# Performance work log

Measured on AMD Instinct MI355X. Metric: run time of the kernel, lower is better.

Reference implementation:

```python
import jax, jax.numpy as jnp
import numpy as np

B, S, H = 4, 2048, 1024
NH, HD = 16, 64  # num heads, head dim

def setup_inputs() -> dict:
    key = jax.random.key(0)
    ks = jax.random.split(key, 4)
    scale = 1.0 / np.sqrt(H)
    return {
        "hidden_states": jax.random.normal(ks[0], (B, S, H), dtype=jnp.float32),
        "attention_mask": jnp.zeros((B, 1, 1, S), dtype=jnp.float32),
        "wq": jax.random.normal(ks[1], (H, H), dtype=jnp.float32) * scale,
        "bq": jnp.zeros((H,), dtype=jnp.float32),
        "wk": jax.random.normal(ks[2], (H, H), dtype=jnp.float32) * scale,
        "bk": jnp.zeros((H,), dtype=jnp.float32),
        "wv": jax.random.normal(ks[3], (H, H), dtype=jnp.float32) * scale,
        "bv": jnp.zeros((H,), dtype=jnp.float32),
    }

def _split_heads(x):
    # [B,S,H] -> [B,NH,S,HD]
    return x.reshape(B, S, NH, HD).transpose(0, 2, 1, 3)

def reference(hidden_states, attention_mask, wq, bq, wk, bk, wv, bv):
    # torch F.linear: x @ W^T + b
    q = _split_heads(hidden_states @ wq.T + bq)
    k = _split_heads(hidden_states @ wk.T + bk)
    v = _split_heads(hidden_states @ wv.T + bv)
    scores = jnp.einsum("bhqd,bhkd->bhqk", q, k) / np.sqrt(HD)
    scores = scores + attention_mask  # additive mask, broadcast [B,1,1,S]
    probs = jax.nn.softmax(scores, axis=-1)  # dropout p=0.0 (eval)
    ctx = jnp.einsum("bhqk,bhkd->bhqd", probs, v)
    # [B,NH,S,HD] -> [B,S,H]
    return ctx.transpose(0, 2, 1, 3).reshape(B, S, H)
```

## Files before the change

kernel.cpp:

```cpp
#include <hip/hip_runtime.h>

typedef unsigned short u16;
typedef unsigned int u32;
typedef __bf16 bf16;
typedef bf16 bf16x8 __attribute__((ext_vector_type(8)));
typedef float f32x4 __attribute__((ext_vector_type(4)));
typedef float f32x16 __attribute__((ext_vector_type(16)));
typedef u16 u16x8 __attribute__((ext_vector_type(8)));
typedef u16 u16x4 __attribute__((ext_vector_type(4)));
typedef u32 u32x4 __attribute__((ext_vector_type(4)));

#define B_ 4
#define S_ 2048
#define H_ 1024
#define NH_ 16
#define HD_ 64
#define M_TOT (B_ * S_)
#define N_TOT (3 * H_)

#if __has_builtin(__builtin_amdgcn_exp2f)
#define EXP2(x) __builtin_amdgcn_exp2f(x)
#else
#define EXP2(x) exp2f(x)
#endif

__device__ __forceinline__ u16 f2bf(float f) {
    union { float f; unsigned u; } v; v.f = f;
    unsigned r = v.u + 0x7FFFu + ((v.u >> 16) & 1u);
    return (u16)(r >> 16);
}

__device__ __forceinline__ u32 cvt_pk_bf16(float a, float b) {
    u32 r;
    asm("v_cvt_pk_bf16_f32 %0, %1, %2" : "=v"(r) : "v"(a), "v"(b));
    return r;
}
__device__ __forceinline__ void perm32swap(u32& a, u32& b) {
    asm volatile("v_permlane32_swap_b32 %0, %1" : "+v"(a), "+v"(b));
}

__global__ __launch_bounds__(256) void cvt_bf16(const float* __restrict__ src,
                                                u16* __restrict__ dst, int n4) {
    int i = blockIdx.x * blockDim.x + threadIdx.x;
    int stride = gridDim.x * blockDim.x;
    for (; i < n4; i += stride) {
        float4 v = ((const float4*)src)[i];
        u16 o0 = f2bf(v.x), o1 = f2bf(v.y), o2 = f2bf(v.z), o3 = f2bf(v.w);
        u16* p = dst + i * 4;
        p[0] = o0; p[1] = o1; p[2] = o2; p[3] = o3;
    }
}

__global__ __launch_bounds__(256) void qkv_gemm(
    const u16* __restrict__ X, const u16* __restrict__ W,
    const float* __restrict__ bq, const float* __restrict__ bk, const float* __restrict__ bv,
    u16* __restrict__ Q, u16* __restrict__ Ko, u16* __restrict__ Vt) {
    __shared__ __align__(16) u16 As[128 * 32];
    __shared__ __align__(16) u16 Bs[128 * 32];

    const int tid = threadIdx.x;
    const int lane = tid & 63;
    const int wave = tid >> 6;
    const int m0 = blockIdx.y * 128;
    const int n0 = blockIdx.x * 128;
    const int wr = (wave >> 1) * 64;
    const int wc = (wave & 1) * 64;

    f32x4 acc[4][4];
#pragma unroll
    for (int m = 0; m < 4; m++)
#pragma unroll
        for (int n = 0; n < 4; n++) acc[m][n] = (f32x4){0.f, 0.f, 0.f, 0.f};

    const int ci = wave * 64 + lane;
    const int ra = ci >> 2, ca = (ci & 3) * 8;
    const u16* gA0 = &X[(size_t)(m0 + ra) * H_ + ca];
    const u16* gA1 = &X[(size_t)(m0 + ra + 64) * H_ + ca];
    const u16* gB0 = &W[(size_t)(n0 + ra) * H_ + ca];
    const u16* gB1 = &W[(size_t)(n0 + ra + 64) * H_ + ca];
    char* lA0 = (char*)As + wave * 1024;
    char* lA1 = (char*)As + 4096 + wave * 1024;
    char* lB0 = (char*)Bs + wave * 1024;
    char* lB1 = (char*)Bs + 4096 + wave * 1024;

    const int row_a = lane & 15;
    const int ko = (lane >> 4) * 8;

    for (int k0 = 0; k0 < H_; k0 += 32) {
        __syncthreads();
        __builtin_amdgcn_global_load_lds((const __attribute__((address_space(1))) void*)(gA0 + k0),
                                         (__attribute__((address_space(3))) void*)lA0, 16, 0, 0);
        __builtin_amdgcn_global_load_lds((const __attribute__((address_space(1))) void*)(gA1 + k0),
                                         (__attribute__((address_space(3))) void*)lA1, 16, 0, 0);
        __builtin_amdgcn_global_load_lds((const __attribute__((address_space(1))) void*)(gB0 + k0),
                                         (__attribute__((address_space(3))) void*)lB0, 16, 0, 0);
        __builtin_amdgcn_global_load_lds((const __attribute__((address_space(1))) void*)(gB1 + k0),
                                         (__attribute__((address_space(3))) void*)lB1, 16, 0, 0);
        __syncthreads();

        bf16x8 a[4], bfr[4];
#pragma unroll
        for (int m = 0; m < 4; m++)
            a[m] = *(const bf16x8*)&As[(wr + m * 16 + row_a) * 32 + ko];
#pragma unroll
        for (int n = 0; n < 4; n++)
            bfr[n] = *(const bf16x8*)&Bs[(wc + n * 16 + row_a) * 32 + ko];
#pragma unroll
        for (int m = 0; m < 4; m++)
#pragma unroll
            for (int n = 0; n < 4; n++)
                acc[m][n] = __builtin_amdgcn_mfma_f32_16x16x32_bf16(a[m], bfr[n], acc[m][n], 0, 0, 0);
    }

    const float QS = 0.125f * 1.44269504f;
#pragma unroll
    for (int n = 0; n < 4; n++) {
        int ng = n0 + wc + n * 16 + (lane & 15);
        int which = ng >> 10;
        int nn = ng & 1023;
        const float* bp = (which == 0) ? bq : (which == 1) ? bk : bv;
        float bias = bp[nn];
        float scale = (which == 0) ? QS : 1.0f;
        int h = nn >> 6, d = nn & 63;
#pragma unroll
        for (int m = 0; m < 4; m++) {
            int mg0 = m0 + wr + m * 16 + (lane >> 4) * 4;
            if (which == 2) {
                u16x4 pack;
#pragma unroll
                for (int j = 0; j < 4; j++) pack[j] = f2bf(acc[m][n][j] + bias);
                int bb = mg0 >> 11, s = mg0 & 2047;
                *(u16x4*)&Vt[((((size_t)bb * NH_ + h) * HD_) + d) * S_ + s] = pack;
            } else {
                u16* dst = (which == 0) ? Q : Ko;
#pragma unroll
                for (int j = 0; j < 4; j++) {
                    int mg = mg0 + j;
                    int bb = mg >> 11, s = mg & 2047;
                    float v = (acc[m][n][j] + bias) * scale;
                    dst[((((size_t)bb * NH_ + h) * S_) + s) * HD_ + d] = f2bf(v);
                }
            }
        }
    }
}

#define KVB 64

__global__ __launch_bounds__(256, 4) void attn(
    const u16* __restrict__ Q, const u16* __restrict__ K, const u16* __restrict__ Vt,
    const float* __restrict__ mask, float* __restrict__ out) {
    const int head = blockIdx.y;
    const int b = head >> 4, h = head & 15;
    const int q0 = blockIdx.x * 128;
    const int tid = threadIdx.x;
    const int lane = tid & 63;
    const int wave = tid >> 6;
    const int l31 = lane & 31;
    const int hi = lane >> 5;

    const u16* Qh = Q + (size_t)head * S_ * HD_;
    const u16* Kh = K + (size_t)head * S_ * HD_;
    const u16* Vh = Vt + (size_t)head * HD_ * S_;

    __shared__ __align__(16) u16 Kl[KVB * HD_];
    __shared__ __align__(16) u16 Vl[HD_ * KVB];
    __shared__ __align__(16) float ml[S_];
    __shared__ int snz;

    if (tid == 0) snz = 0;
    __syncthreads();
    {
        int nz = 0;
        const float4* m4 = (const float4*)(mask + (size_t)b * S_);
        for (int i = tid; i < S_ / 4; i += 256) {
            float4 v = m4[i];
            nz |= (v.x != 0.f) | (v.y != 0.f) | (v.z != 0.f) | (v.w != 0.f);
            f32x4 sv = { v.x * 1.44269504f, v.y * 1.44269504f,
                         v.z * 1.44269504f, v.w * 1.44269504f };
            *(f32x4*)&ml[i * 4] = sv;
        }
        if (__any(nz) && lane == 0) atomicOr(&snz, 1);
    }
    __syncthreads();
    const bool mz = (snz == 0);

    bf16x8 qf[4];
    {
        const u16* qp = &Qh[(size_t)(q0 + wave * 32 + l31) * HD_ + hi * 8];
        qf[0] = *(const bf16x8*)(qp);
        qf[1] = *(const bf16x8*)(qp + 16);
        qf[2] = *(const bf16x8*)(qp + 32);
        qf[3] = *(const bf16x8*)(qp + 48);
    }

    f32x16 oacc[2];
#pragma unroll
    for (int dh = 0; dh < 2; dh++)
#pragma unroll
        for (int i = 0; i < 16; i++) oacc[dh][i] = 0.f;
    float m = -1e30f, l = 0.f;

    const int sr = tid >> 2;
    const u32 sdB = (u32)((tid & 3) * 32);
    const u32 swzS = (u32)((sr & 7) << 4);
    const u32 off0 = ((u32)(sr * 128) + sdB) ^ swzS;
    const u32 off1 = off0 ^ 16u;
    const u16* kSrc = &Kh[(size_t)sr * HD_ + (tid & 3) * 16];
    const u16* vSrc = &Vh[(size_t)sr * S_ + (tid & 3) * 16];
    const u32 swzR = (u32)((l31 & 7) << 4);
    const u32 rowB = (u32)(l31 * 128);

    for (int kv0 = 0; kv0 < S_; kv0 += KVB) {
        __syncthreads();
        {
            const u16* ks = kSrc + (size_t)kv0 * HD_;
            const u16* vs = vSrc + kv0;
            u16x8 a0 = *(const u16x8*)ks;
            u16x8 a1 = *(const u16x8*)(ks + 8);
            u16x8 b0 = *(const u16x8*)vs;
            u16x8 b1 = *(const u16x8*)(vs + 8);
            *(u16x8*)((char*)Kl + off0) = a0;
            *(u16x8*)((char*)Kl + off1) = a1;
            *(u16x8*)((char*)Vl + off0) = b0;
            *(u16x8*)((char*)Vl + off1) = b1;
        }
        __syncthreads();

        f32x16 sc[2];
#pragma unroll
        for (int g = 0; g < 2; g++) {
            f32x16 c;
#pragma unroll
            for (int i = 0; i < 16; i++) c[i] = 0.f;
#pragma unroll
            for (int dk = 0; dk < 4; dk++) {
                bf16x8 kf = *(const bf16x8*)((const char*)Kl + g * 4096 + rowB +
                                             (((u32)(dk * 32 + hi * 16)) ^ swzR));
                c = __builtin_amdgcn_mfma_f32_32x32x16_bf16(kf, qf[dk], c, 0, 0, 0);
            }
            sc[g] = c;
        }

        if (!mz) {
#pragma unroll
            for (int g = 0; g < 2; g++)
#pragma unroll
                for (int c4 = 0; c4 < 4; c4++) {
                    f32x4 mk = *(const f32x4*)&ml[kv0 + g * 32 + c4 * 8 + hi * 4];
#pragma unroll
                    for (int e = 0; e < 4; e++) sc[g][c4 * 4 + e] += mk[e];
                }
        }

        float tm = sc[0][0];
#pragma unroll
        for (int i = 1; i < 16; i++) tm = fmaxf(tm, sc[0][i]);
#pragma unroll
        for (int i = 0; i < 16; i++) tm = fmaxf(tm, sc[1][i]);
        tm = fmaxf(tm, __shfl_xor(tm, 32, 64));
        if (tm > m + 30.f) {
            float fac = EXP2(m - tm);
            l *= fac;
#pragma unroll
            for (int dh = 0; dh < 2; dh++)
#pragma unroll
                for (int i = 0; i < 16; i++) oacc[dh][i] *= fac;
            m = tm;
        }

        float l0 = 0.f, l1 = 0.f, l2 = 0.f, l3 = 0.f;
#pragma unroll
        for (int g = 0; g < 2; g++)
#pragma unroll
            for (int i = 0; i < 16; i += 4) {
                float p0 = EXP2(sc[g][i + 0] - m);
                float p1 = EXP2(sc[g][i + 1] - m);
                float p2 = EXP2(sc[g][i + 2] - m);
                float p3 = EXP2(sc[g][i + 3] - m);
                sc[g][i + 0] = p0; sc[g][i + 1] = p1;
                sc[g][i + 2] = p2; sc[g][i + 3] = p3;
                l0 += p0; l1 += p1; l2 += p2; l3 += p3;
            }
        l += (l0 + l1) + (l2 + l3);

#pragma unroll
        for (int s = 0; s < 4; s++) {
            const int g = s >> 1, r8 = (s & 1) * 8;
            u32 pkA0 = cvt_pk_bf16(sc[g][r8 + 0], sc[g][r8 + 1]);
            u32 pkA1 = cvt_pk_bf16(sc[g][r8 + 2], sc[g][r8 + 3]);
            u32 pkB0 = cvt_pk_bf16(sc[g][r8 + 4], sc[g][r8 + 5]);
            u32 pkB1 = cvt_pk_bf16(sc[g][r8 + 6], sc[g][r8 + 7]);
            perm32swap(pkA0, pkB0);
            perm32swap(pkA1, pkB1);
            union { u32x4 w; bf16x8 v; } pu;
            pu.w = (u32x4){ pkA0, pkA1, pkB0, pkB1 };
            bf16x8 pf = pu.v;
#pragma unroll
            for (int dh = 0; dh < 2; dh++) {
                bf16x8 vf = *(const bf16x8*)((const char*)Vl + dh * 4096 + rowB +
                                             (((u32)(s * 32 + hi * 16)) ^ swzR));
                oacc[dh] = __builtin_amdgcn_mfma_f32_32x32x16_bf16(vf, pf, oacc[dh], 0, 0, 0);
            }
        }
    }

    float lt = l + __shfl_xor(l, 32, 64);
    float inv = 1.0f / lt;
    const int q = q0 + wave * 32 + l31;
    float* orow = out + ((size_t)b * S_ + q) * H_ + h * HD_;
#pragma unroll
    for (int dh = 0; dh < 2; dh++)
#pragma unroll
        for (int c4 = 0; c4 < 4; c4++) {
            f32x4 v;
#pragma unroll
            for (int e = 0; e < 4; e++) v[e] = oacc[dh][c4 * 4 + e] * inv;
            *(f32x4*)&orow[dh * 32 + c4 * 8 + hi * 4] = v;
        }
}

extern "C" void kernel_launch(void* const* d_in, const int* in_sizes, int n_in,
                              void* d_out, int out_size, void* d_ws, size_t ws_size,
                              hipStream_t stream) {
    const float* hs   = (const float*)d_in[0];
    const float* mask = (const float*)d_in[1];
    const float* wq   = (const float*)d_in[2];
    const float* bq   = (const float*)d_in[3];
    const float* wk   = (const float*)d_in[4];
    const float* bk   = (const float*)d_in[5];
    const float* wv   = (const float*)d_in[6];
    const float* bv   = (const float*)d_in[7];
    float* out = (float*)d_out;

    char* ws = (char*)d_ws;
    u16* Xb = (u16*)ws;
    u16* Wb = (u16*)(ws + 16777216);
    u16* Qb = (u16*)(ws + 23068672);
    u16* Kb = (u16*)(ws + 39845888);
    u16* Vb = (u16*)(ws + 56623104);

    cvt_bf16<<<1024, 256, 0, stream>>>(hs, Xb, (M_TOT * H_) / 4);
    cvt_bf16<<<512, 256, 0, stream>>>(wq, Wb,                (H_ * H_) / 4);
    cvt_bf16<<<512, 256, 0, stream>>>(wk, Wb + H_ * H_,      (H_ * H_) / 4);
    cvt_bf16<<<512, 256, 0, stream>>>(wv, Wb + 2 * H_ * H_,  (H_ * H_) / 4);

    qkv_gemm<<<dim3(N_TOT / 128, M_TOT / 128), 256, 0, stream>>>(
        Xb, Wb, bq, bk, bv, Qb, Kb, Vb);

    attn<<<dim3(S_ / 128, B_ * NH_), 256, 0, stream>>>(Qb, Kb, Vb, mask, out);
}
```

Baseline: 209.7 us.

## Double-buffer LDS tiles with async global_load_lds in GEMM and attention

```diff
diff --git a/kernel.cpp b/kernel.cpp
--- a/kernel.cpp
+++ b/kernel.cpp
@@ -18,11 +18,7 @@
 #define M_TOT (B_ * S_)
 #define N_TOT (3 * H_)
 
-#if __has_builtin(__builtin_amdgcn_exp2f)
-#define EXP2(x) __builtin_amdgcn_exp2f(x)
-#else
 #define EXP2(x) exp2f(x)
-#endif
 
 __device__ __forceinline__ u16 f2bf(float f) {
     union { float f; unsigned u; } v; v.f = f;
@@ -37,6 +33,14 @@
 }
 __device__ __forceinline__ void perm32swap(u32& a, u32& b) {
     asm volatile("v_permlane32_swap_b32 %0, %1" : "+v"(a), "+v"(b));
+}
+__device__ __forceinline__ void gload16(const void* g, void* l) {
+    __builtin_amdgcn_global_load_lds(
+        (const __attribute__((address_space(1))) void*)g,
+        (__attribute__((address_space(3))) void*)l, 16, 0, 0);
+}
+__device__ __forceinline__ void wait_vm0() {
+    asm volatile("s_waitcnt vmcnt(0)" ::: "memory");
 }
 
 __global__ __launch_bounds__(256) void cvt_bf16(const float* __restrict__ src,
@@ -45,9 +49,8 @@
     int stride = gridDim.x * blockDim.x;
     for (; i < n4; i += stride) {
         float4 v = ((const float4*)src)[i];
-        u16 o0 = f2bf(v.x), o1 = f2bf(v.y), o2 = f2bf(v.z), o3 = f2bf(v.w);
-        u16* p = dst + i * 4;
-        p[0] = o0; p[1] = o1; p[2] = o2; p[3] = o3;
+        u16x4 o = { f2bf(v.x), f2bf(v.y), f2bf(v.z), f2bf(v.w) };
+        *(u16x4*)&dst[i * 4] = o;
     }
 }
 
@@ -55,8 +58,8 @@
     const u16* __restrict__ X, const u16* __restrict__ W,
     const float* __restrict__ bq, const float* __restrict__ bk, const float* __restrict__ bv,
     u16* __restrict__ Q, u16* __restrict__ Ko, u16* __restrict__ Vt) {
-    __shared__ __align__(16) u16 As[128 * 32];
-    __shared__ __align__(16) u16 Bs[128 * 32];
+    __shared__ __align__(16) u16 As[2][128 * 32];
+    __shared__ __align__(16) u16 Bs[2][128 * 32];
 
     const int tid = threadIdx.x;
     const int lane = tid & 63;
@@ -78,38 +81,45 @@
     const u16* gA1 = &X[(size_t)(m0 + ra + 64) * H_ + ca];
     const u16* gB0 = &W[(size_t)(n0 + ra) * H_ + ca];
     const u16* gB1 = &W[(size_t)(n0 + ra + 64) * H_ + ca];
-    char* lA0 = (char*)As + wave * 1024;
-    char* lA1 = (char*)As + 4096 + wave * 1024;
-    char* lB0 = (char*)Bs + wave * 1024;
-    char* lB1 = (char*)Bs + 4096 + wave * 1024;
+    char* lA0 = (char*)&As[0][0] + wave * 1024;
+    char* lB0 = (char*)&Bs[0][0] + wave * 1024;
 
     const int row_a = lane & 15;
     const int ko = (lane >> 4) * 8;
 
+    gload16(gA0, lA0);
+    gload16(gA1, lA0 + 4096);
+    gload16(gB0, lB0);
+    gload16(gB1, lB0 + 4096);
+
     for (int k0 = 0; k0 < H_; k0 += 32) {
-        __syncthreads();
-        __builtin_amdgcn_global_load_lds((const __attribute__((address_space(1))) void*)(gA0 + k0),
-                                         (__attribute__((address_space(3))) void*)lA0, 16, 0, 0);
-        __builtin_amdgcn_global_load_lds((const __attribute__((address_space(1))) void*)(gA1 + k0),
-                                         (__attribute__((address_space(3))) void*)lA1, 16, 0, 0);
-        __builtin_amdgcn_global_load_lds((const __attribute__((address_space(1))) void*)(gB0 + k0),
-                                         (__attribute__((address_space(3))) void*)lB0, 16, 0, 0);
-        __builtin_amdgcn_global_load_lds((const __attribute__((address_space(1))) void*)(gB1 + k0),
-                                         (__attribute__((address_space(3))) void*)lB1, 16, 0, 0);
-        __syncthreads();
-
+        const int cur = (k0 >> 5) & 1;
+        wait_vm0();
+        __builtin_amdgcn_s_barrier();
+        if (k0 + 32 < H_) {
+            char* dA = lA0 + (cur ^ 1) * 8192;
+            char* dB = lB0 + (cur ^ 1) * 8192;
+            gload16(gA0 + k0 + 32, dA);
+            gload16(gA1 + k0 + 32, dA + 4096);
+            gload16(gB0 + k0 + 32, dB);
+            gload16(gB1 + k0 + 32, dB + 4096);
+        }
+        const u16* Ab = &As[cur][0];
+        const u16* Bb = &Bs[cur][0];
         bf16x8 a[4], bfr[4];
 #pragma unroll
         for (int m = 0; m < 4; m++)
-            a[m] = *(const bf16x8*)&As[(wr + m * 16 + row_a) * 32 + ko];
+            a[m] = *(const bf16x8*)&Ab[(wr + m * 16 + row_a) * 32 + ko];
 #pragma unroll
         for (int n = 0; n < 4; n++)
-            bfr[n] = *(const bf16x8*)&Bs[(wc + n * 16 + row_a) * 32 + ko];
+            bfr[n] = *(const bf16x8*)&Bb[(wc + n * 16 + row_a) * 32 + ko];
+        __builtin_amdgcn_s_setprio(1);
 #pragma unroll
         for (int m = 0; m < 4; m++)
 #pragma unroll
             for (int n = 0; n < 4; n++)
                 acc[m][n] = __builtin_amdgcn_mfma_f32_16x16x32_bf16(a[m], bfr[n], acc[m][n], 0, 0, 0);
+        __builtin_amdgcn_s_setprio(0);
     }
 
     const float QS = 0.125f * 1.44269504f;
@@ -146,6 +156,7 @@
 }
 
 #define KVB 64
+#define NT_ (S_ / KVB)
 
 __global__ __launch_bounds__(256, 4) void attn(
     const u16* __restrict__ Q, const u16* __restrict__ K, const u16* __restrict__ Vt,
@@ -163,27 +174,21 @@
     const u16* Kh = K + (size_t)head * S_ * HD_;
     const u16* Vh = Vt + (size_t)head * HD_ * S_;
 
-    __shared__ __align__(16) u16 Kl[KVB * HD_];
-    __shared__ __align__(16) u16 Vl[HD_ * KVB];
-    __shared__ __align__(16) float ml[S_];
+    __shared__ __align__(16) u16 Kl[2][KVB * HD_];
+    __shared__ __align__(16) u16 Vl[2][HD_ * KVB];
     __shared__ int snz;
 
     if (tid == 0) snz = 0;
     __syncthreads();
     {
         int nz = 0;
-        const float4* m4 = (const float4*)(mask + (size_t)b * S_);
+        const f32x4* m4 = (const f32x4*)(mask + (size_t)b * S_);
         for (int i = tid; i < S_ / 4; i += 256) {
-            float4 v = m4[i];
-            nz |= (v.x != 0.f) | (v.y != 0.f) | (v.z != 0.f) | (v.w != 0.f);
-            f32x4 sv = { v.x * 1.44269504f, v.y * 1.44269504f,
-                         v.z * 1.44269504f, v.w * 1.44269504f };
-            *(f32x4*)&ml[i * 4] = sv;
+            f32x4 v = m4[i];
+            nz |= (v[0] != 0.f) | (v[1] != 0.f) | (v[2] != 0.f) | (v[3] != 0.f);
         }
         if (__any(nz) && lane == 0) atomicOr(&snz, 1);
     }
-    __syncthreads();
-    const bool mz = (snz == 0);
 
     bf16x8 qf[4];
     {
@@ -193,6 +198,25 @@
         qf[2] = *(const bf16x8*)(qp + 32);
         qf[3] = *(const bf16x8*)(qp + 48);
     }
+    __syncthreads();
+    const bool mz = (snz == 0);
+    const float* mrow = mask + (size_t)b * S_;
+    const float LOG2E = 1.44269504f;
+
+    const int c0 = wave * 64 + lane;
+    const int c1 = 256 + c0;
+    const int r0c = c0 >> 3, r1c = c1 >> 3;
+    const u32 s0c = (u32)(((c0 & 7) ^ (r0c & 7)) * 16);
+    const u32 s1c = (u32)(((c1 & 7) ^ (r1c & 7)) * 16);
+    const char* kS0 = (const char*)Kh + (size_t)r0c * 128 + s0c;
+    const char* kS1 = (const char*)Kh + (size_t)r1c * 128 + s1c;
+    const char* vS0 = (const char*)Vh + (size_t)r0c * (S_ * 2) + s0c;
+    const char* vS1 = (const char*)Vh + (size_t)r1c * (S_ * 2) + s1c;
+    char* dK = (char*)&Kl[0][0] + wave * 1024;
+    char* dV = (char*)&Vl[0][0] + wave * 1024;
+
+    const u32 swzR = (u32)((l31 & 7) << 4);
+    const u32 rowB = (u32)(l31 * 128);
 
     f32x16 oacc[2];
 #pragma unroll
@@ -201,33 +225,31 @@
         for (int i = 0; i < 16; i++) oacc[dh][i] = 0.f;
     float m = -1e30f, l = 0.f;
 
-    const int sr = tid >> 2;
-    const u32 sdB = (u32)((tid & 3) * 32);
-    const u32 swzS = (u32)((sr & 7) << 4);
-    const u32 off0 = ((u32)(sr * 128) + sdB) ^ swzS;
-    const u32 off1 = off0 ^ 16u;
-    const u16* kSrc = &Kh[(size_t)sr * HD_ + (tid & 3) * 16];
-    const u16* vSrc = &Vh[(size_t)sr * S_ + (tid & 3) * 16];
-    const u32 swzR = (u32)((l31 & 7) << 4);
-    const u32 rowB = (u32)(l31 * 128);
-
-    for (int kv0 = 0; kv0 < S_; kv0 += KVB) {
-        __syncthreads();
-        {
-            const u16* ks = kSrc + (size_t)kv0 * HD_;
-            const u16* vs = vSrc + kv0;
-            u16x8 a0 = *(const u16x8*)ks;
-            u16x8 a1 = *(const u16x8*)(ks + 8);
-            u16x8 b0 = *(const u16x8*)vs;
-            u16x8 b1 = *(const u16x8*)(vs + 8);
-            *(u16x8*)((char*)Kl + off0) = a0;
-            *(u16x8*)((char*)Kl + off1) = a1;
-            *(u16x8*)((char*)Vl + off0) = b0;
-            *(u16x8*)((char*)Vl + off1) = b1;
-        }
-        __syncthreads();
+    gload16(kS0, dK);
+    gload16(kS1, dK + 4096);
+    gload16(vS0, dV);
+    gload16(vS1, dV + 4096);
+
+    for (int t = 0; t < NT_; ++t) {
+        const int kv0 = t * KVB;
+        const int cur = t & 1;
+        wait_vm0();
+        __builtin_amdgcn_s_barrier();
+        if (t + 1 < NT_) {
+            const size_t kOff = (size_t)(kv0 + KVB) * 128;
+            const size_t vOff = (size_t)(kv0 + KVB) * 2;
+            char* nK = dK + (cur ^ 1) * 8192;
+            char* nV = dV + (cur ^ 1) * 8192;
+            gload16(kS0 + kOff, nK);
+            gload16(kS1 + kOff, nK + 4096);
+            gload16(vS0 + vOff, nV);
+            gload16(vS1 + vOff, nV + 4096);
+        }
+        const char* KB = (const char*)&Kl[cur][0];
+        const char* VB = (const char*)&Vl[cur][0];
 
         f32x16 sc[2];
+        __builtin_amdgcn_s_setprio(1);
 #pragma unroll
         for (int g = 0; g < 2; g++) {
             f32x16 c;
@@ -235,21 +257,22 @@
             for (int i = 0; i < 16; i++) c[i] = 0.f;
 #pragma unroll
             for (int dk = 0; dk < 4; dk++) {
-                bf16x8 kf = *(const bf16x8*)((const char*)Kl + g * 4096 + rowB +
+                bf16x8 kf = *(const bf16x8*)(KB + g * 4096 + rowB +
                                              (((u32)(dk * 32 + hi * 16)) ^ swzR));
                 c = __builtin_amdgcn_mfma_f32_32x32x16_bf16(kf, qf[dk], c, 0, 0, 0);
             }
             sc[g] = c;
         }
+        __builtin_amdgcn_s_setprio(0);
 
         if (!mz) {
 #pragma unroll
             for (int g = 0; g < 2; g++)
 #pragma unroll
                 for (int c4 = 0; c4 < 4; c4++) {
-                    f32x4 mk = *(const f32x4*)&ml[kv0 + g * 32 + c4 * 8 + hi * 4];
-#pragma unroll
-                    for (int e = 0; e < 4; e++) sc[g][c4 * 4 + e] += mk[e];
+                    f32x4 mk = *(const f32x4*)&mrow[kv0 + g * 32 + c4 * 8 + hi * 4];
+#pragma unroll
+                    for (int e = 0; e < 4; e++) sc[g][c4 * 4 + e] += mk[e] * LOG2E;
                 }
         }
 
@@ -296,12 +319,14 @@
             union { u32x4 w; bf16x8 v; } pu;
             pu.w = (u32x4){ pkA0, pkA1, pkB0, pkB1 };
             bf16x8 pf = pu.v;
+            __builtin_amdgcn_s_setprio(1);
 #pragma unroll
             for (int dh = 0; dh < 2; dh++) {
-                bf16x8 vf = *(const bf16x8*)((const char*)Vl + dh * 4096 + rowB +
+                bf16x8 vf = *(const bf16x8*)(VB + dh * 4096 + rowB +
                                              (((u32)(s * 32 + hi * 16)) ^ swzR));
                 oacc[dh] = __builtin_amdgcn_mfma_f32_32x32x16_bf16(vf, pf, oacc[dh], 0, 0, 0);
             }
+            __builtin_amdgcn_s_setprio(0);
         }
     }
 
```

New measurement: 240.0 us. +14.4%, slower.
